# Performance work log

Hardware: AMD Instinct MI355X
Metric: run time of the kernel (lower is better)

Reference implementation:

```python
import jax, jax.numpy as jnp
import numpy as np

N_NODES = 100000
N_EDGES = 3200000
F_IN, F_HID, F_OUT = 128, 16, 8


def _gcn_norm(edge_index, n):
    """Add self-loops and compute symmetric GCN normalization coefficients."""
    loops = jnp.arange(n, dtype=edge_index.dtype)
    src = jnp.concatenate([edge_index[0], loops])
    dst = jnp.concatenate([edge_index[1], loops])
    deg = jax.ops.segment_sum(jnp.ones_like(dst, dtype=jnp.float32), dst,
                              num_segments=n)
    dinv = jnp.where(deg > 0, jax.lax.rsqrt(deg), 0.0)
    norm = dinv[src] * dinv[dst]  # [E + N]
    return src, dst, norm


def _gcn_conv(x, W, b, src, dst, norm, n):
    h = x @ W                                  # [N, F_out] transform first (F_out small)
    msg = h[src] * norm[:, None]               # gather + scale  [E+N, F_out]
    return jax.ops.segment_sum(msg, dst, num_segments=n) + b


def setup_inputs() -> dict:
    key = jax.random.key(0)
    k1, k2, k3, k4, k5 = jax.random.split(key, 5)
    x = jax.random.normal(k1, (N_NODES, F_IN), dtype=jnp.float32)
    edge_index = jax.random.randint(k2, (2, N_EDGES), 0, N_NODES, dtype=jnp.int64)
    # Glorot-style init for GCNConv weights, zero bias (PyG default)
    s1 = (6.0 / (F_IN + F_HID)) ** 0.5
    s2 = (6.0 / (F_HID + F_OUT)) ** 0.5
    W1 = jax.random.uniform(k3, (F_IN, F_HID), jnp.float32, -s1, s1)
    W2 = jax.random.uniform(k4, (F_HID, F_OUT), jnp.float32, -s2, s2)
    b1 = jnp.zeros((F_HID,), jnp.float32)
    b2 = jnp.zeros((F_OUT,), jnp.float32)
    return {"x": x, "edge_index": edge_index, "W1": W1, "b1": b1,
            "W2": W2, "b2": b2}


def reference(x, edge_index, W1, b1, W2, b2):
    n = x.shape[0]
    src, dst, norm = _gcn_norm(edge_index, n)
    h = _gcn_conv(x, W1, b1, src, dst, norm, n)
    h = jax.nn.relu(h)
    # F.dropout(training=False) in eval mode -> identity
    h = _gcn_conv(h, W2, b2, src, dst, norm, n)
    return jax.nn.log_softmax(h, axis=1)
```

## Files before the change

### kernel.cpp

```cpp
#include <hip/hip_runtime.h>
#include <math.h>

#define F_IN 128
#define F_HID 16
#define F_OUT 8
#define BSHIFT 7
#define BNODES 128
#define MAXNB 1024
#define CHUNK 8192

__device__ inline unsigned bf16rn(float x) {
    unsigned u = __float_as_uint(x);
    u += 0x7fffu + ((u >> 16) & 1u);
    return u >> 16;
}
__device__ inline float b2f(unsigned h) { return __uint_as_float(h << 16); }


__global__ void k_zero(int* __restrict__ p, int m) {
    int i = blockIdx.x * blockDim.x + threadIdx.x;
    if (i < m) p[i] = 0;
}


__global__ __launch_bounds__(256) void k_hist(const int* __restrict__ dst,
                                              int* __restrict__ bucket_cnt,
                                              int e, int nb) {
    __shared__ int sh[MAXNB];
    int t = threadIdx.x;
    for (int i = t; i < nb; i += 256) sh[i] = 0;
    __syncthreads();
    int stride = gridDim.x * 256;
    for (int i = blockIdx.x * 256 + t; i < e; i += stride)
        atomicAdd(&sh[dst[i] >> BSHIFT], 1);
    __syncthreads();
    for (int i = t; i < nb; i += 256)
        if (sh[i]) atomicAdd(&bucket_cnt[i], sh[i]);
}


__global__ __launch_bounds__(256) void k_scan(const int* __restrict__ bucket_cnt,
                                              int* __restrict__ base,
                                              int* __restrict__ cursor,
                                              int* __restrict__ row_ptr, int nb, int e, int n) {
    __shared__ int sh[256];
    int t = threadIdx.x;
    int v[4], s = 0;
#pragma unroll
    for (int q = 0; q < 4; ++q) {
        int i = t * 4 + q;
        v[q] = (i < nb) ? bucket_cnt[i] : 0;
        s += v[q];
    }
    sh[t] = s;
    __syncthreads();
    for (int off = 1; off < 256; off <<= 1) {
        int x = (t >= off) ? sh[t - off] : 0;
        __syncthreads();
        sh[t] += x;
        __syncthreads();
    }
    int run = (t > 0) ? sh[t - 1] : 0;
#pragma unroll
    for (int q = 0; q < 4; ++q) {
        int i = t * 4 + q;
        if (i < nb) { base[i] = run; cursor[i] = run; }
        run += v[q];
    }
    if (t == 0) { base[nb] = e; row_ptr[n] = e; }
}


__global__ __launch_bounds__(1024) void k_bucket(const int* __restrict__ src,
                                                 const int* __restrict__ dst,
                                                 int* __restrict__ cursor,
                                                 int* __restrict__ ebuf, int e, int nb) {
    __shared__ int hist[MAXNB];
    __shared__ int ofs[MAXNB];
    int t = threadIdx.x;
    int beg = blockIdx.x * CHUNK;
    int end = min(beg + CHUNK, e);
    for (int i = t; i < nb; i += 1024) hist[i] = 0;
    __syncthreads();
    for (int i = beg + t; i < end; i += 1024)
        atomicAdd(&hist[dst[i] >> BSHIFT], 1);
    __syncthreads();
    for (int i = t; i < nb; i += 1024)
        ofs[i] = hist[i] ? atomicAdd(&cursor[i], hist[i]) : 0;
    __syncthreads();
    for (int i = beg + t; i < end; i += 1024) {
        int s = src[i], d = dst[i];
        int pos = atomicAdd(&ofs[d >> BSHIFT], 1);
        ebuf[pos] = (s << BSHIFT) | (d & (BNODES - 1));
    }
}


__global__ __launch_bounds__(256) void k_sort(const int* __restrict__ ebuf,
                                              const int* __restrict__ base,
                                              int* __restrict__ csr,
                                              int* __restrict__ row_ptr,
                                              float* __restrict__ dinv, int n) {
    __shared__ int cnt[BNODES];
    __shared__ int sh[BNODES];
    __shared__ int cur[BNODES];
    int b = blockIdx.x, t = threadIdx.x;
    if (t < BNODES) cnt[t] = 0;
    __syncthreads();
    int st = base[b], en = base[b + 1];
    for (int i = st + t; i < en; i += 256)
        atomicAdd(&cnt[ebuf[i] & (BNODES - 1)], 1);
    __syncthreads();
    if (t < BNODES) sh[t] = cnt[t];
    __syncthreads();
    for (int off = 1; off < BNODES; off <<= 1) {
        int x = (t >= off && t < BNODES) ? sh[t - off] : 0;
        __syncthreads();
        if (t < BNODES) sh[t] += x;
        __syncthreads();
    }
    if (t < BNODES) {
        int excl = (t > 0) ? sh[t - 1] : 0;
        int node = b * BNODES + t;
        if (node < n) {
            row_ptr[node] = st + excl;
            dinv[node] = rsqrtf((float)cnt[t] + 1.0f);
        }
        cur[t] = st + excl;
    }
    __syncthreads();
    for (int i = st + t; i < en; i += 256) {
        int ep = ebuf[i];
        int pos = atomicAdd(&cur[ep & (BNODES - 1)], 1);
        csr[pos] = ep >> BSHIFT;
    }
}


__global__ __launch_bounds__(256) void k_gemm1(const float* __restrict__ x,
                                               const float* __restrict__ W1,
                                               const float* __restrict__ dinv,
                                               unsigned short* __restrict__ g1b, int n) {
    int t = threadIdx.x;
    int h = __builtin_amdgcn_readfirstlane(t >> 7);
    int row = blockIdx.x * 128 + (t & 127);
    if (row >= n) return;
    const float4* xr = (const float4*)(x + (size_t)row * F_IN);
    const float* Wh = W1 + h * 8;
    float acc[8] = {0, 0, 0, 0, 0, 0, 0, 0};
#pragma unroll 8
    for (int kq = 0; kq < 32; ++kq) {
        float4 xv = xr[kq];
        int k0 = kq * 4;
#pragma unroll
        for (int j = 0; j < 8; ++j) {
            acc[j] = fmaf(xv.x, Wh[(k0 + 0) * F_HID + j], acc[j]);
            acc[j] = fmaf(xv.y, Wh[(k0 + 1) * F_HID + j], acc[j]);
            acc[j] = fmaf(xv.z, Wh[(k0 + 2) * F_HID + j], acc[j]);
            acc[j] = fmaf(xv.w, Wh[(k0 + 3) * F_HID + j], acc[j]);
        }
    }
    float di = dinv[row];
    unsigned pk[4];
#pragma unroll
    for (int j = 0; j < 4; ++j) {
        unsigned lo = bf16rn(acc[2 * j] * di);
        unsigned hi = bf16rn(acc[2 * j + 1] * di);
        pk[j] = lo | (hi << 16);
    }
    ((uint4*)g1b)[(size_t)row * 2 + h] = make_uint4(pk[0], pk[1], pk[2], pk[3]);
}


__global__ __launch_bounds__(256) void k_gather1(const int* __restrict__ row_ptr,
                                                 const int* __restrict__ csr,
                                                 const float* __restrict__ dinv,
                                                 const unsigned short* __restrict__ g1b,
                                                 const float* __restrict__ b1,
                                                 const float* __restrict__ W2,
                                                 float* __restrict__ g2, int n) {
    int t = threadIdx.x;
    int node = blockIdx.x * 128 + (t >> 1);
    int q = t & 1;
    if (node >= n) return;
    int st = row_ptr[node], en = row_ptr[node + 1];
    const uint4* rows = (const uint4*)g1b;
    float a[8];
    uint4 v = rows[(size_t)node * 2 + q];
    a[0] = b2f(v.x & 0xffffu); a[1] = b2f(v.x >> 16);
    a[2] = b2f(v.y & 0xffffu); a[3] = b2f(v.y >> 16);
    a[4] = b2f(v.z & 0xffffu); a[5] = b2f(v.z >> 16);
    a[6] = b2f(v.w & 0xffffu); a[7] = b2f(v.w >> 16);
    int k = st;
    for (; k + 2 <= en; k += 2) {
        int s0 = csr[k], s1 = csr[k + 1];
        uint4 v0 = rows[(size_t)s0 * 2 + q];
        uint4 v1 = rows[(size_t)s1 * 2 + q];
        a[0] += b2f(v0.x & 0xffffu) + b2f(v1.x & 0xffffu);
        a[1] += b2f(v0.x >> 16)     + b2f(v1.x >> 16);
        a[2] += b2f(v0.y & 0xffffu) + b2f(v1.y & 0xffffu);
        a[3] += b2f(v0.y >> 16)     + b2f(v1.y >> 16);
        a[4] += b2f(v0.z & 0xffffu) + b2f(v1.z & 0xffffu);
        a[5] += b2f(v0.z >> 16)     + b2f(v1.z >> 16);
        a[6] += b2f(v0.w & 0xffffu) + b2f(v1.w & 0xffffu);
        a[7] += b2f(v0.w >> 16)     + b2f(v1.w >> 16);
    }
    if (k < en) {
        int s0 = csr[k];
        uint4 v0 = rows[(size_t)s0 * 2 + q];
        a[0] += b2f(v0.x & 0xffffu); a[1] += b2f(v0.x >> 16);
        a[2] += b2f(v0.y & 0xffffu); a[3] += b2f(v0.y >> 16);
        a[4] += b2f(v0.z & 0xffffu); a[5] += b2f(v0.z >> 16);
        a[6] += b2f(v0.w & 0xffffu); a[7] += b2f(v0.w >> 16);
    }
    float di = dinv[node];
    float h_own[8], h_oth[8];
#pragma unroll
    for (int j = 0; j < 8; ++j)
        h_own[j] = fmaxf(di * a[j] + b1[q * 8 + j], 0.0f);
#pragma unroll
    for (int j = 0; j < 8; ++j) h_oth[j] = __shfl_xor(h_own[j], 1);
    float flo[8], fhi[8];
#pragma unroll
    for (int j = 0; j < 8; ++j) {
        flo[j] = (q == 0) ? h_own[j] : h_oth[j];
        fhi[j] = (q == 0) ? h_oth[j] : h_own[j];
    }
    int jj0 = q * 4;
    float o0 = 0, o1 = 0, o2 = 0, o3 = 0;
#pragma unroll
    for (int kk = 0; kk < 16; ++kk) {
        float hk = (kk < 8) ? flo[kk] : fhi[kk - 8];
        const float* wr = &W2[kk * F_OUT + jj0];
        o0 = fmaf(hk, wr[0], o0);
        o1 = fmaf(hk, wr[1], o1);
        o2 = fmaf(hk, wr[2], o2);
        o3 = fmaf(hk, wr[3], o3);
    }
    *(float4*)&g2[(size_t)node * F_OUT + jj0] =
        make_float4(o0 * di, o1 * di, o2 * di, o3 * di);
}


__global__ __launch_bounds__(256) void k_gather2(const int* __restrict__ row_ptr,
                                                 const int* __restrict__ csr,
                                                 const float* __restrict__ dinv,
                                                 const float* __restrict__ g2,
                                                 const float* __restrict__ b2,
                                                 float* __restrict__ out, int n) {
    int t = threadIdx.x;
    int node = blockIdx.x * 128 + (t >> 1);
    int q = t & 1;
    if (node >= n) return;
    int st = row_ptr[node], en = row_ptr[node + 1];
    const float4* rows = (const float4*)g2;
    float4 s4 = rows[(size_t)node * 2 + q];
    float a0 = s4.x, a1 = s4.y, a2 = s4.z, a3 = s4.w;
    int k = st;
    for (; k + 2 <= en; k += 2) {
        int s0 = csr[k], s1 = csr[k + 1];
        float4 v0 = rows[(size_t)s0 * 2 + q];
        float4 v1 = rows[(size_t)s1 * 2 + q];
        a0 += v0.x + v1.x; a1 += v0.y + v1.y;
        a2 += v0.z + v1.z; a3 += v0.w + v1.w;
    }
    if (k < en) {
        float4 v0 = rows[(size_t)csr[k] * 2 + q];
        a0 += v0.x; a1 += v0.y; a2 += v0.z; a3 += v0.w;
    }
    float di = dinv[node];
    float v0 = di * a0 + b2[q * 4 + 0];
    float v1 = di * a1 + b2[q * 4 + 1];
    float v2 = di * a2 + b2[q * 4 + 2];
    float v3 = di * a3 + b2[q * 4 + 3];
    float m = fmaxf(fmaxf(v0, v1), fmaxf(v2, v3));
    m = fmaxf(m, __shfl_xor(m, 1));
    float ss = expf(v0 - m) + expf(v1 - m) + expf(v2 - m) + expf(v3 - m);
    ss += __shfl_xor(ss, 1);
    float ls = m + logf(ss);
    *(float4*)&out[(size_t)node * F_OUT + q * 4] =
        make_float4(v0 - ls, v1 - ls, v2 - ls, v3 - ls);
}


extern "C" void kernel_launch(void* const* d_in, const int* in_sizes, int n_in,
                              void* d_out, int out_size, void* d_ws, size_t ws_size,
                              hipStream_t stream) {
    const float* x  = (const float*)d_in[0];
    const int*   ei = (const int*)d_in[1];
    const float* W1 = (const float*)d_in[2];
    const float* b1 = (const float*)d_in[3];
    const float* W2 = (const float*)d_in[4];
    const float* b2 = (const float*)d_in[5];
    float* out = (float*)d_out;

    const int n = in_sizes[0] / F_IN;
    const int e = in_sizes[1] / 2;
    const int* src = ei;
    const int* dst = ei + e;
    const int nb = (n + BNODES - 1) / BNODES;

    char* w = (char*)d_ws;
    float* dinv         = (float*)w; w += (size_t)n * 4;
    int* ebuf           = (int*)w;   w += (size_t)e * 4;
    int* csr            = (int*)w;   w += (size_t)e * 4;
    int* row_ptr        = (int*)w;   w += (size_t)(n + 4) * 4;
    int* bucket_cnt     = (int*)w;   w += (size_t)(nb + 4) * 4;
    int* base           = (int*)w;   w += (size_t)(nb + 4) * 4;
    int* cursor         = (int*)w;   w += (size_t)(nb + 4) * 4;
    w = (char*)(((size_t)w + 15) & ~(size_t)15);
    unsigned short* g1b = (unsigned short*)w; w += (size_t)n * F_HID * 2;
    w = (char*)(((size_t)w + 15) & ~(size_t)15);
    float* g2           = (float*)w; w += (size_t)n * F_OUT * 4;

    k_zero<<<(nb + 255) / 256, 256, 0, stream>>>(bucket_cnt, nb);
    k_hist<<<256, 256, 0, stream>>>(dst, bucket_cnt, e, nb);
    k_scan<<<1, 256, 0, stream>>>(bucket_cnt, base, cursor, row_ptr, nb, e, n);
    k_bucket<<<(e + CHUNK - 1) / CHUNK, 1024, 0, stream>>>(src, dst, cursor, ebuf, e, nb);
    k_sort<<<nb, 256, 0, stream>>>(ebuf, base, csr, row_ptr, dinv, n);
    k_gemm1<<<(n + 127) / 128, 256, 0, stream>>>(x, W1, dinv, g1b, n);
    k_gather1<<<(n + 127) / 128, 256, 0, stream>>>(row_ptr, csr, dinv, g1b, b1, W2, g2, n);
    k_gather2<<<(n + 127) / 128, 256, 0, stream>>>(row_ptr, csr, dinv, g2, b2, out, n);
}
```

Baseline: 278.9 us.

## Stage bucket scatter and CSR sort through shared memory for coalesced writes

The bucketing kernel now sorts each 8192-edge chunk locally in shared memory by bucket, using a block-wide prefix scan, and then writes to ebuf in contiguous runs instead of scattering each edge with its own global offset. The per-bucket CSR sort likewise builds its output in a shared buffer and copies it out linearly, falling back to the old scatter when a bucket has more than 8192 edges. The goal is to turn random global writes into coalesced ones. In exchange it uses much more LDS per block, which can reduce occupancy, and adds extra barriers and scan steps.

```diff
diff --git a/kernel.cpp b/kernel.cpp
--- a/kernel.cpp
+++ b/kernel.cpp
@@ -8,6 +8,7 @@
 #define BNODES 128
 #define MAXNB 1024
 #define CHUNK 8192
+#define SORTBUF 8192
 
 __device__ inline unsigned bf16rn(float x) {
     unsigned u = __float_as_uint(x);
@@ -76,23 +77,58 @@
                                                  int* __restrict__ cursor,
                                                  int* __restrict__ ebuf, int e, int nb) {
     __shared__ int hist[MAXNB];
-    __shared__ int ofs[MAXNB];
+    __shared__ int lofs[MAXNB];
+    __shared__ int delta[MAXNB];
+    __shared__ int sorted[CHUNK];
+    __shared__ unsigned short bkt[CHUNK];
     int t = threadIdx.x;
     int beg = blockIdx.x * CHUNK;
     int end = min(beg + CHUNK, e);
+    int cn = end - beg;
     for (int i = t; i < nb; i += 1024) hist[i] = 0;
     __syncthreads();
-    for (int i = beg + t; i < end; i += 1024)
-        atomicAdd(&hist[dst[i] >> BSHIFT], 1);
-    __syncthreads();
-    for (int i = t; i < nb; i += 1024)
-        ofs[i] = hist[i] ? atomicAdd(&cursor[i], hist[i]) : 0;
-    __syncthreads();
-    for (int i = beg + t; i < end; i += 1024) {
-        int s = src[i], d = dst[i];
-        int pos = atomicAdd(&ofs[d >> BSHIFT], 1);
-        ebuf[pos] = (s << BSHIFT) | (d & (BNODES - 1));
-    }
+    int myw[8], mybr[8];
+#pragma unroll
+    for (int u = 0; u < 8; ++u) {
+        int i = beg + t + u * 1024;
+        if (i < end) {
+            int s = src[i], d = dst[i];
+            int b = d >> BSHIFT;
+            myw[u] = (s << BSHIFT) | (d & (BNODES - 1));
+            int r = atomicAdd(&hist[b], 1);
+            mybr[u] = (b << 16) | r;
+        }
+    }
+    __syncthreads();
+    int v = (t < nb) ? hist[t] : 0;
+    lofs[t] = v;
+    __syncthreads();
+    for (int off = 1; off < 1024; off <<= 1) {
+        int x = (t >= off) ? lofs[t - off] : 0;
+        __syncthreads();
+        lofs[t] += x;
+        __syncthreads();
+    }
+    int excl = lofs[t] - v;
+    lofs[t] = excl;
+    if (t < nb) {
+        int g = v ? atomicAdd(&cursor[t], v) : 0;
+        delta[t] = g - excl;
+    }
+    __syncthreads();
+#pragma unroll
+    for (int u = 0; u < 8; ++u) {
+        int i = beg + t + u * 1024;
+        if (i < end) {
+            int b = mybr[u] >> 16, r = mybr[u] & 0xffff;
+            int p = lofs[b] + r;
+            sorted[p] = myw[u];
+            bkt[p] = (unsigned short)b;
+        }
+    }
+    __syncthreads();
+    for (int j = t; j < cn; j += 1024)
+        ebuf[delta[bkt[j]] + j] = sorted[j];
 }
 
 
@@ -104,10 +140,12 @@
     __shared__ int cnt[BNODES];
     __shared__ int sh[BNODES];
     __shared__ int cur[BNODES];
+    __shared__ int buf[SORTBUF];
     int b = blockIdx.x, t = threadIdx.x;
     if (t < BNODES) cnt[t] = 0;
     __syncthreads();
     int st = base[b], en = base[b + 1];
+    int cn = en - st;
     for (int i = st + t; i < en; i += 256)
         atomicAdd(&cnt[ebuf[i] & (BNODES - 1)], 1);
     __syncthreads();
@@ -126,13 +164,25 @@
             row_ptr[node] = st + excl;
             dinv[node] = rsqrtf((float)cnt[t] + 1.0f);
         }
-        cur[t] = st + excl;
-    }
-    __syncthreads();
-    for (int i = st + t; i < en; i += 256) {
-        int ep = ebuf[i];
-        int pos = atomicAdd(&cur[ep & (BNODES - 1)], 1);
-        csr[pos] = ep >> BSHIFT;
+        cur[t] = excl;
+    }
+    __syncthreads();
+    if (cn <= SORTBUF) {
+        for (int i = st + t; i < en; i += 256) {
+            int ep = ebuf[i];
+            int p = atomicAdd(&cur[ep & (BNODES - 1)], 1);
+            buf[p] = ep >> BSHIFT;
+        }
+        __syncthreads();
+        for (int j = t; j < cn; j += 256) csr[st + j] = buf[j];
+    } else {
+        if (t < BNODES) cur[t] += st;
+        __syncthreads();
+        for (int i = st + t; i < en; i += 256) {
+            int ep = ebuf[i];
+            int pos = atomicAdd(&cur[ep & (BNODES - 1)], 1);
+            csr[pos] = ep >> BSHIFT;
+        }
     }
 }
 
```

New measurement: 252.0 us. 1.11x faster.
